# Kernel optimization log

Hardware: AMD Instinct MI355X
Metric: run time of the kernel (lower is better)

Reference implementation:

```python
import jax, jax.numpy as jnp
import numpy as np

B, N, D, H = 2, 2048, 1024, 16
HD = D // H  # head dim = 64
SCALING = (D / H) ** 0.5  # sqrt(64) = 8
EPS = 1e-5


def setup_inputs() -> dict:
    key = jax.random.key(0)
    k1, k2, k3 = jax.random.split(key, 3)
    return {
        "z": jax.random.normal(k1, (B, N, D), dtype=jnp.float32),
        "ln_scale": jnp.ones((D,), dtype=jnp.float32),
        "ln_bias": jnp.zeros((D,), dtype=jnp.float32),
        "w_qkv": jax.random.normal(k2, (D, 3 * D), dtype=jnp.float32) * (D ** -0.5),
        "w_proj": jax.random.normal(k3, (D, D), dtype=jnp.float32) * (D ** -0.5),
        "b_proj": jnp.zeros((D,), dtype=jnp.float32),
    }


def reference(z, ln_scale, ln_bias, w_qkv, w_proj, b_proj):
    b, n, d = z.shape
    # LayerNorm (pre-norm)
    mu = jnp.mean(z, axis=-1, keepdims=True)
    var = jnp.mean(jnp.square(z - mu), axis=-1, keepdims=True)
    zn = (z - mu) / jnp.sqrt(var + EPS) * ln_scale + ln_bias
    # QKV projection: [b, n, 3D]
    qkv = zn @ w_qkv
    # einops 'b n (h d qkv_n) -> qkv_n b h n d': qkv index is innermost
    qkv5 = qkv.reshape(b, n, H, HD, 3)  # [b, n, h, d, 3]
    q = jnp.transpose(qkv5[..., 0], (0, 2, 1, 3))  # [b, h, n, d]
    k = jnp.transpose(qkv5[..., 1], (0, 2, 1, 3))
    v = jnp.transpose(qkv5[..., 2], (0, 2, 1, 3))
    # Attention: scores scaled AFTER the matmul, as in the source
    scores = jnp.einsum('bhqd,bhkd->bhqk', q, k) / SCALING
    att = jax.nn.softmax(scores, axis=-1)
    out = jnp.einsum('bhal,bhlv->bhav', att, v)  # [b, h, n, d]
    out = jnp.transpose(out, (0, 2, 1, 3)).reshape(b, n, d)  # merge heads
    out = out @ w_proj + b_proj  # projection (dropout p=0)
    return z + out
```

## Files before the change

kernel.cpp:

```cpp
#include <hip/hip_runtime.h>
#include <stdint.h>
#include <math.h>

typedef unsigned short u16;
typedef float f32x4 __attribute__((ext_vector_type(4)));
typedef __bf16 bf16x8 __attribute__((ext_vector_type(8)));

__device__ __forceinline__ u16 f2bf(float f) {
    union { float f; uint32_t u; } c; c.f = f;
    return (u16)((c.u + 0x7FFFu + ((c.u >> 16) & 1u)) >> 16);
}

__device__ __forceinline__ void gload_lds16(const void* g, void* l) {
    __builtin_amdgcn_global_load_lds(
        (const __attribute__((address_space(1))) unsigned int*)g,
        (__attribute__((address_space(3))) unsigned int*)l, 16, 0, 0);
}

__global__ __launch_bounds__(256) void prep_kernel(const float* __restrict__ z,
                                                   const float* __restrict__ sc,
                                                   const float* __restrict__ bs,
                                                   const float* __restrict__ w_qkv,
                                                   const float* __restrict__ w_proj,
                                                   u16* __restrict__ zn,
                                                   u16* __restrict__ wqkvT,
                                                   u16* __restrict__ wprojT) {
    __shared__ float t[32][33];
    const int tid = threadIdx.x;
    const int bid = blockIdx.x;

    if (bid < 4096) {
        float* red = &t[0][0];
        const int row = bid;
        const float4 v = ((const float4*)(z + (size_t)row * 1024))[tid];
        float s = v.x + v.y + v.z + v.w;
        #pragma unroll
        for (int off = 32; off > 0; off >>= 1) s += __shfl_xor(s, off);
        if ((tid & 63) == 0) red[tid >> 6] = s;
        __syncthreads();
        const float mean = (red[0] + red[1] + red[2] + red[3]) * (1.0f / 1024.0f);
        const float dx = v.x - mean, dy = v.y - mean, dz = v.z - mean, dw = v.w - mean;
        float q = dx * dx + dy * dy + dz * dz + dw * dw;
        #pragma unroll
        for (int off = 32; off > 0; off >>= 1) q += __shfl_xor(q, off);
        if ((tid & 63) == 0) red[4 + (tid >> 6)] = q;
        __syncthreads();
        const float var = (red[4] + red[5] + red[6] + red[7]) * (1.0f / 1024.0f);
        const float rstd = rsqrtf(var + 1e-5f);
        const float4 scv = ((const float4*)sc)[tid];
        const float4 bsv = ((const float4*)bs)[tid];
        const u16 o0 = f2bf(dx * rstd * scv.x + bsv.x);
        const u16 o1 = f2bf(dy * rstd * scv.y + bsv.y);
        const u16 o2 = f2bf(dz * rstd * scv.z + bsv.z);
        const u16 o3 = f2bf(dw * rstd * scv.w + bsv.w);
        uint2 pk;
        pk.x = (uint32_t)o0 | ((uint32_t)o1 << 16);
        pk.y = (uint32_t)o2 | ((uint32_t)o3 << 16);
        *(uint2*)&zn[(size_t)row * 1024 + tid * 4] = pk;
        return;
    }

    const float* in;
    u16* out;
    int K, N, permute, bx, by;
    if (bid < 4096 + 3072) {
        const int r = bid - 4096;
        in = w_qkv; out = wqkvT; K = 1024; N = 3072; permute = 1;
        bx = r % 96; by = r / 96;
    } else {
        const int r = bid - 4096 - 3072;
        in = w_proj; out = wprojT; K = 1024; N = 1024; permute = 0;
        bx = r % 32; by = r / 32;
    }
    const int j = tid & 31, i0 = tid >> 5;
    const int kb = by * 32, nb = bx * 32;
    #pragma unroll
    for (int p = 0; p < 4; ++p) {
        int r = i0 + p * 8;
        t[r][j] = in[(size_t)(kb + r) * N + nb + j];
    }
    __syncthreads();
    #pragma unroll
    for (int p = 0; p < 4; ++p) {
        int r = i0 + p * 8;
        int c = nb + r;
        int np = c;
        if (permute) {
            int h = c / 192, rem = c - h * 192;
            int d = rem / 3, s = rem - d * 3;
            np = s * 1024 + h * 64 + d;
        }
        out[(size_t)np * K + kb + j] = f2bf(t[j][r]);
    }
}

__global__ __launch_bounds__(256, 3) void gemm_qkv(const u16* __restrict__ A,
                                                   const u16* __restrict__ Bt,
                                                   u16* __restrict__ qbuf,
                                                   u16* __restrict__ kbuf,
                                                   u16* __restrict__ vT) {
    __shared__ __align__(16) u16 sm[64 * 136];
    u16* const As = sm;
    u16* const Bs = sm + 4096;
    const int tid = threadIdx.x;
    const int wave = tid >> 6, lane = tid & 63;
    const int quad = lane >> 4, l16 = lane & 15;
    const int wm = (wave >> 1) * 64, wn = (wave & 1) * 64;
    const int row0 = blockIdx.x * 128, col0 = blockIdx.y * 128;
    const int gr = lane >> 2, gc = (lane & 3) * 8;
    f32x4 acc[4][4] = {};
    for (int kt = 0; kt < 1024; kt += 32) {
        __syncthreads();
        #pragma unroll
        for (int i = 0; i < 2; ++i) {
            const int rb = wave * 16 + i * 64;
            gload_lds16(&A[(size_t)(row0 + rb + gr) * 1024 + kt + gc], &As[rb * 32]);
            gload_lds16(&Bt[(size_t)(col0 + rb + gr) * 1024 + kt + gc], &Bs[rb * 32]);
        }
        __syncthreads();
        bf16x8 ax[4], bx[4];
        #pragma unroll
        for (int t = 0; t < 4; ++t) {
            ax[t] = *(const bf16x8*)&As[(wm + t * 16 + l16) * 32 + quad * 8];
            bx[t] = *(const bf16x8*)&Bs[(wn + t * 16 + l16) * 32 + quad * 8];
        }
        #pragma unroll
        for (int mt = 0; mt < 4; ++mt)
            #pragma unroll
            for (int nt = 0; nt < 4; ++nt)
                acc[mt][nt] = __builtin_amdgcn_mfma_f32_16x16x32_bf16(ax[mt], bx[nt], acc[mt][nt], 0, 0, 0);
    }
    const int s = col0 >> 10;
    if (s < 2) {
        u16* const dst = (s == 0) ? qbuf : kbuf;
        const float scl = (s == 0) ? 0.125f * 1.44269504088896f : 1.0f;
        #pragma unroll
        for (int mt = 0; mt < 4; ++mt) {
            #pragma unroll
            for (int nt = 0; nt < 4; ++nt) {
                #pragma unroll
                for (int e = 0; e < 4; ++e) {
                    const int row = row0 + wm + mt * 16 + quad * 4 + e;
                    const int col = col0 + wn + nt * 16 + l16;
                    const int b = row >> 11, n = row & 2047;
                    const int h = (col >> 6) & 15, d = col & 63;
                    dst[((size_t)(b * 16 + h) * 2048 + n) * 64 + d] = f2bf(acc[mt][nt][e] * scl);
                }
            }
        }
    } else {
        const int b = row0 >> 11, n0 = row0 & 2047;
        const int h0 = (col0 >> 6) & 15;
        for (int hh = 0; hh < 2; ++hh) {
            __syncthreads();
            if ((wave & 1) == hh) {
                #pragma unroll
                for (int mt = 0; mt < 4; ++mt) {
                    const int rl = wm + mt * 16 + quad * 4;
                    #pragma unroll
                    for (int nt = 0; nt < 4; ++nt) {
                        const int cl = nt * 16 + l16;
                        u16 tmp[4];
                        #pragma unroll
                        for (int e = 0; e < 4; ++e) tmp[e] = f2bf(acc[mt][nt][e]);
                        *(uint2*)&sm[cl * 136 + rl] = *(const uint2*)tmp;
                    }
                }
            }
            __syncthreads();
            const int bh = b * 16 + h0 + hh;
            #pragma unroll
            for (int pass = 0; pass < 4; ++pass) {
                const int chunk = pass * 256 + tid;
                const int d = chunk >> 4;
                const int nc = chunk & 15;
                const uint4 vv = *(const uint4*)&sm[d * 136 + nc * 8];
                *(uint4*)&vT[((size_t)bh * 64 + d) * 2048 + n0 + nc * 8] = vv;
            }
        }
    }
}

__global__ __launch_bounds__(512, 2) void attn_kernel(const u16* __restrict__ qb,
                                                      const u16* __restrict__ kb,
                                                      const u16* __restrict__ vT,
                                                      u16* __restrict__ att_out) {
    __shared__ __align__(16) char lds_raw[71680];
    u16* const smem0 = (u16*)lds_raw;
    const int tid = threadIdx.x;
    const int wave = tid >> 6, lane = tid & 63;
    const int quad = lane >> 4, l16 = lane & 15;
    const int kw = wave & 3, qw = wave >> 2;
    const int qt = blockIdx.x, bh = blockIdx.y;
    const int b = bh >> 4, h = bh & 15;

    bf16x8 qf[4][2];
    #pragma unroll
    for (int g = 0; g < 4; ++g) {
        const u16* qrow = &qb[(size_t)(bh * 2048 + qt * 128 + qw * 64 + g * 16 + l16) * 64];
        qf[g][0] = *(const bf16x8*)&qrow[quad * 8];
        qf[g][1] = *(const bf16x8*)&qrow[32 + quad * 8];
    }

    const u16* ksrc[2];
    const u16* vsrc[2];
    int kofs[2], vofs[2];
    #pragma unroll
    for (int j = 0; j < 2; ++j) {
        const int p = 8 * wave + 64 * j + (lane >> 3);
        const int kr = (p & 0x60) | ((p & 12) << 1) | ((p & 16) >> 2) | (p & 3);
        const int gk = (lane & 7) ^ (p & 7);
        ksrc[j] = kb + ((size_t)bh * 2048 + kr) * 64 + gk * 8;
        kofs[j] = (8 * wave + 64 * j) * 64;
        const int d = 4 * wave + 32 * j + (lane >> 4);
        const int gv = (lane & 15) ^ (d & 15);
        vsrc[j] = vT + ((size_t)bh * 64 + d) * 2048 + gv * 8;
        vofs[j] = 8192 + (4 * wave + 32 * j) * 128;
    }

    f32x4 o[4][4] = {};
    f32x4 l[4] = {};
    bf16x8 ones;
    #pragma unroll
    for (int i = 0; i < 8; ++i) ones[i] = (__bf16)1.0f;

    #pragma unroll
    for (int j = 0; j < 2; ++j) {
        gload_lds16(ksrc[j], smem0 + kofs[j]);
        gload_lds16(vsrc[j], smem0 + vofs[j]);
        ksrc[j] += 128 * 64;
        vsrc[j] += 128;
    }

    for (int kt = 0; kt < 16; ++kt) {
        __syncthreads();
        if (kt < 15) {
            u16* nb_ = smem0 + ((kt + 1) & 1) * 16384;
            #pragma unroll
            for (int j = 0; j < 2; ++j) {
                gload_lds16(ksrc[j], nb_ + kofs[j]);
                gload_lds16(vsrc[j], nb_ + vofs[j]);
                ksrc[j] += 128 * 64;
                vsrc[j] += 128;
            }
        }
        const u16* Ks = smem0 + (kt & 1) * 16384;
        const u16* Vs = Ks + 8192;

        f32x4 s[2][4] = {};
        __builtin_amdgcn_s_setprio(1);
        #pragma unroll
        for (int mtl = 0; mtl < 2; ++mtl) {
            const int r = kw * 32 + mtl * 16 + l16;
            const bf16x8 k0 = *(const bf16x8*)&Ks[r * 64 + (((quad) ^ (r & 7)) << 3)];
            const bf16x8 k1 = *(const bf16x8*)&Ks[r * 64 + (((quad + 4) ^ (r & 7)) << 3)];
            #pragma unroll
            for (int g = 0; g < 4; ++g) {
                s[mtl][g] = __builtin_amdgcn_mfma_f32_16x16x32_bf16(k0, qf[g][0], s[mtl][g], 0, 0, 0);
                s[mtl][g] = __builtin_amdgcn_mfma_f32_16x16x32_bf16(k1, qf[g][1], s[mtl][g], 0, 0, 0);
            }
        }
        __builtin_amdgcn_s_setprio(0);

        bf16x8 ap[4];
        #pragma unroll
        for (int g = 0; g < 4; ++g)
            #pragma unroll
            for (int mtl = 0; mtl < 2; ++mtl)
                #pragma unroll
                for (int e = 0; e < 4; ++e)
                    ap[g][mtl * 4 + e] = (__bf16)__builtin_amdgcn_exp2f(s[mtl][g][e]);

        __builtin_amdgcn_s_setprio(1);
        #pragma unroll
        for (int vt = 0; vt < 4; ++vt) {
            const int dd = vt * 16 + l16;
            const bf16x8 vf = *(const bf16x8*)&Vs[dd * 128 + (((kw * 4 + quad) ^ l16) << 3)];
            #pragma unroll
            for (int g = 0; g < 4; ++g)
                o[g][vt] = __builtin_amdgcn_mfma_f32_16x16x32_bf16(ap[g], vf, o[g][vt], 0, 0, 0);
        }
        #pragma unroll
        for (int g = 0; g < 4; ++g)
            l[g] = __builtin_amdgcn_mfma_f32_16x16x32_bf16(ap[g], ones, l[g], 0, 0, 0);
        __builtin_amdgcn_s_setprio(0);
    }

    float* const red = (float*)lds_raw;
    float* const lred = (float*)(lds_raw + 69632);
    #pragma unroll
    for (int qg = 0; qg < 2; ++qg) {
        __syncthreads();
        if (qw == qg) {
            #pragma unroll
            for (int g = 0; g < 4; ++g) {
                #pragma unroll
                for (int vt = 0; vt < 4; ++vt)
                    #pragma unroll
                    for (int e = 0; e < 4; ++e)
                        red[(kw * 64 + g * 16 + quad * 4 + e) * 68 + vt * 16 + l16] = o[g][vt][e];
                if (l16 == 0) {
                    #pragma unroll
                    for (int e = 0; e < 4; ++e)
                        lred[kw * 64 + g * 16 + quad * 4 + e] = l[g][e];
                }
            }
        }
        __syncthreads();
        #pragma unroll
        for (int rep = 0; rep < 2; ++rep) {
            const int idx = rep * 512 + tid;
            const int q = idx >> 4, dc = idx & 15;
            const f32x4 a0 = *(const f32x4*)&red[(0 * 64 + q) * 68 + dc * 4];
            const f32x4 a1 = *(const f32x4*)&red[(1 * 64 + q) * 68 + dc * 4];
            const f32x4 a2 = *(const f32x4*)&red[(2 * 64 + q) * 68 + dc * 4];
            const f32x4 a3 = *(const f32x4*)&red[(3 * 64 + q) * 68 + dc * 4];
            const f32x4 ss = a0 + a1 + a2 + a3;
            const float li = lred[q] + lred[64 + q] + lred[128 + q] + lred[192 + q];
            const float inv = 1.0f / li;
            u16 pk[4];
            #pragma unroll
            for (int e = 0; e < 4; ++e) pk[e] = f2bf(ss[e] * inv);
            const int qrow = qt * 128 + qg * 64 + q;
            *(uint2*)&att_out[(size_t)(b * 2048 + qrow) * 1024 + h * 64 + dc * 4] = *(const uint2*)pk;
        }
    }
}

__global__ __launch_bounds__(256) void gemm_proj(const u16* __restrict__ A,
                                                 const u16* __restrict__ Bt,
                                                 const float* __restrict__ bias,
                                                 const float* __restrict__ z,
                                                 float* __restrict__ out) {
    __shared__ __align__(16) u16 As[64 * 32];
    __shared__ __align__(16) u16 Bs[128 * 32];
    const int tid = threadIdx.x;
    const int wave = tid >> 6, lane = tid & 63;
    const int quad = lane >> 4, l16 = lane & 15;
    const int wm = (wave >> 1) * 32, wn = (wave & 1) * 64;
    const int row0 = blockIdx.x * 64, col0 = blockIdx.y * 128;
    const int gr = lane >> 2, gc = (lane & 3) * 8;
    f32x4 acc[2][4] = {};
    for (int kt = 0; kt < 1024; kt += 32) {
        __syncthreads();
        gload_lds16(&A[(size_t)(row0 + wave * 16 + gr) * 1024 + kt + gc], &As[(wave * 16) * 32]);
        #pragma unroll
        for (int i = 0; i < 2; ++i) {
            const int rb = wave * 16 + i * 64;
            gload_lds16(&Bt[(size_t)(col0 + rb + gr) * 1024 + kt + gc], &Bs[rb * 32]);
        }
        __syncthreads();
        bf16x8 ax[2], bx[4];
        #pragma unroll
        for (int t = 0; t < 2; ++t)
            ax[t] = *(const bf16x8*)&As[(wm + t * 16 + l16) * 32 + quad * 8];
        #pragma unroll
        for (int t = 0; t < 4; ++t)
            bx[t] = *(const bf16x8*)&Bs[(wn + t * 16 + l16) * 32 + quad * 8];
        #pragma unroll
        for (int mt = 0; mt < 2; ++mt)
            #pragma unroll
            for (int nt = 0; nt < 4; ++nt)
                acc[mt][nt] = __builtin_amdgcn_mfma_f32_16x16x32_bf16(ax[mt], bx[nt], acc[mt][nt], 0, 0, 0);
    }
    #pragma unroll
    for (int mt = 0; mt < 2; ++mt) {
        #pragma unroll
        for (int nt = 0; nt < 4; ++nt) {
            #pragma unroll
            for (int e = 0; e < 4; ++e) {
                const int row = row0 + wm + mt * 16 + quad * 4 + e;
                const int col = col0 + wn + nt * 16 + l16;
                out[(size_t)row * 1024 + col] = acc[mt][nt][e] + bias[col] + z[(size_t)row * 1024 + col];
            }
        }
    }
}

extern "C" void kernel_launch(void* const* d_in, const int* in_sizes, int n_in,
                              void* d_out, int out_size, void* d_ws, size_t ws_size,
                              hipStream_t stream) {
    const float* z        = (const float*)d_in[0];
    const float* ln_scale = (const float*)d_in[1];
    const float* ln_bias  = (const float*)d_in[2];
    const float* w_qkv    = (const float*)d_in[3];
    const float* w_proj   = (const float*)d_in[4];
    const float* b_proj   = (const float*)d_in[5];
    float* out = (float*)d_out;

    char* ws = (char*)d_ws;
    u16* zn     = (u16*)(ws);
    u16* wqkvT  = (u16*)(ws + (8u << 20));
    u16* wprojT = (u16*)(ws + (14u << 20));
    u16* qbuf   = (u16*)(ws + (16u << 20));
    u16* kbuf   = (u16*)(ws + (24u << 20));
    u16* vT     = (u16*)(ws + (32u << 20));
    u16* att_o  = (u16*)(ws + (40u << 20));

    prep_kernel<<<dim3(4096 + 3072 + 1024), 256, 0, stream>>>(
        z, ln_scale, ln_bias, w_qkv, w_proj, zn, wqkvT, wprojT);
    gemm_qkv<<<dim3(32, 24), 256, 0, stream>>>(zn, wqkvT, qbuf, kbuf, vT);
    attn_kernel<<<dim3(16, 32), 512, 0, stream>>>(qbuf, kbuf, vT, att_o);
    gemm_proj<<<dim3(64, 8), 256, 0, stream>>>(att_o, wprojT, b_proj, z, out);
}
```

Measured before the change: 180.3 us.

## Enlarge attention query tile to 256 with 2-way KV split and triple buffering

```diff
diff --git a/kernel.cpp b/kernel.cpp
--- a/kernel.cpp
+++ b/kernel.cpp
@@ -185,19 +185,19 @@
                                                       const u16* __restrict__ kb,
                                                       const u16* __restrict__ vT,
                                                       u16* __restrict__ att_out) {
-    __shared__ __align__(16) char lds_raw[71680];
+    __shared__ __align__(16) char lds_raw[98304];
     u16* const smem0 = (u16*)lds_raw;
     const int tid = threadIdx.x;
     const int wave = tid >> 6, lane = tid & 63;
     const int quad = lane >> 4, l16 = lane & 15;
-    const int kw = wave & 3, qw = wave >> 2;
+    const int kw = wave & 1, qw = wave >> 1;
     const int qt = blockIdx.x, bh = blockIdx.y;
     const int b = bh >> 4, h = bh & 15;
 
     bf16x8 qf[4][2];
     #pragma unroll
     for (int g = 0; g < 4; ++g) {
-        const u16* qrow = &qb[(size_t)(bh * 2048 + qt * 128 + qw * 64 + g * 16 + l16) * 64];
+        const u16* qrow = &qb[(size_t)(bh * 2048 + qt * 256 + qw * 64 + g * 16 + l16) * 64];
         qf[g][0] = *(const bf16x8*)&qrow[quad * 8];
         qf[g][1] = *(const bf16x8*)&qrow[32 + quad * 8];
     }
@@ -224,105 +224,105 @@
     #pragma unroll
     for (int i = 0; i < 8; ++i) ones[i] = (__bf16)1.0f;
 
-    #pragma unroll
-    for (int j = 0; j < 2; ++j) {
-        gload_lds16(ksrc[j], smem0 + kofs[j]);
-        gload_lds16(vsrc[j], smem0 + vofs[j]);
-        ksrc[j] += 128 * 64;
-        vsrc[j] += 128;
-    }
+    auto stage = [&](int buf) {
+        u16* dst = smem0 + buf * 16384;
+        #pragma unroll
+        for (int j = 0; j < 2; ++j) {
+            gload_lds16(ksrc[j], dst + kofs[j]);
+            gload_lds16(vsrc[j], dst + vofs[j]);
+            ksrc[j] += 128 * 64;
+            vsrc[j] += 128;
+        }
+    };
+    stage(0);
+    stage(1);
 
     for (int kt = 0; kt < 16; ++kt) {
-        __syncthreads();
-        if (kt < 15) {
-            u16* nb_ = smem0 + ((kt + 1) & 1) * 16384;
-            #pragma unroll
-            for (int j = 0; j < 2; ++j) {
-                gload_lds16(ksrc[j], nb_ + kofs[j]);
-                gload_lds16(vsrc[j], nb_ + vofs[j]);
-                ksrc[j] += 128 * 64;
-                vsrc[j] += 128;
-            }
-        }
-        const u16* Ks = smem0 + (kt & 1) * 16384;
+        if (kt < 15) asm volatile("s_waitcnt vmcnt(4)\n\ts_barrier" ::: "memory");
+        else         asm volatile("s_waitcnt vmcnt(0)\n\ts_barrier" ::: "memory");
+        if (kt <= 13) stage((kt + 2) % 3);
+
+        const u16* Ks = smem0 + (kt % 3) * 16384;
         const u16* Vs = Ks + 8192;
 
-        f32x4 s[2][4] = {};
-        __builtin_amdgcn_s_setprio(1);
-        #pragma unroll
-        for (int mtl = 0; mtl < 2; ++mtl) {
-            const int r = kw * 32 + mtl * 16 + l16;
-            const bf16x8 k0 = *(const bf16x8*)&Ks[r * 64 + (((quad) ^ (r & 7)) << 3)];
-            const bf16x8 k1 = *(const bf16x8*)&Ks[r * 64 + (((quad + 4) ^ (r & 7)) << 3)];
-            #pragma unroll
-            for (int g = 0; g < 4; ++g) {
-                s[mtl][g] = __builtin_amdgcn_mfma_f32_16x16x32_bf16(k0, qf[g][0], s[mtl][g], 0, 0, 0);
-                s[mtl][g] = __builtin_amdgcn_mfma_f32_16x16x32_bf16(k1, qf[g][1], s[mtl][g], 0, 0, 0);
-            }
-        }
-        __builtin_amdgcn_s_setprio(0);
-
-        bf16x8 ap[4];
-        #pragma unroll
-        for (int g = 0; g < 4; ++g)
-            #pragma unroll
-            for (int mtl = 0; mtl < 2; ++mtl)
-                #pragma unroll
-                for (int e = 0; e < 4; ++e)
-                    ap[g][mtl * 4 + e] = (__bf16)__builtin_amdgcn_exp2f(s[mtl][g][e]);
+        bf16x8 ap[4][2];
+        #pragma unroll
+        for (int f = 0; f < 2; ++f) {
+            f32x4 s2[2][4] = {};
+            #pragma unroll
+            for (int m2 = 0; m2 < 2; ++m2) {
+                const int r = kw * 64 + (f * 2 + m2) * 16 + l16;
+                const bf16x8 k0 = *(const bf16x8*)&Ks[r * 64 + ((quad ^ (r & 7)) << 3)];
+                const bf16x8 k1 = *(const bf16x8*)&Ks[r * 64 + (((quad + 4) ^ (r & 7)) << 3)];
+                #pragma unroll
+                for (int g = 0; g < 4; ++g) {
+                    s2[m2][g] = __builtin_amdgcn_mfma_f32_16x16x32_bf16(k0, qf[g][0], s2[m2][g], 0, 0, 0);
+                    s2[m2][g] = __builtin_amdgcn_mfma_f32_16x16x32_bf16(k1, qf[g][1], s2[m2][g], 0, 0, 0);
+                }
+            }
+            #pragma unroll
+            for (int g = 0; g < 4; ++g)
+                #pragma unroll
+                for (int m2 = 0; m2 < 2; ++m2)
+                    #pragma unroll
+                    for (int e = 0; e < 4; ++e)
+                        ap[g][f][m2 * 4 + e] = (__bf16)__builtin_amdgcn_exp2f(s2[m2][g][e]);
+        }
 
         __builtin_amdgcn_s_setprio(1);
         #pragma unroll
         for (int vt = 0; vt < 4; ++vt) {
             const int dd = vt * 16 + l16;
-            const bf16x8 vf = *(const bf16x8*)&Vs[dd * 128 + (((kw * 4 + quad) ^ l16) << 3)];
-            #pragma unroll
-            for (int g = 0; g < 4; ++g)
-                o[g][vt] = __builtin_amdgcn_mfma_f32_16x16x32_bf16(ap[g], vf, o[g][vt], 0, 0, 0);
-        }
-        #pragma unroll
-        for (int g = 0; g < 4; ++g)
-            l[g] = __builtin_amdgcn_mfma_f32_16x16x32_bf16(ap[g], ones, l[g], 0, 0, 0);
+            #pragma unroll
+            for (int f = 0; f < 2; ++f) {
+                const int c = kw * 2 + f;
+                const bf16x8 vf = *(const bf16x8*)&Vs[dd * 128 + (((c * 4 + quad) ^ l16) << 3)];
+                #pragma unroll
+                for (int g = 0; g < 4; ++g)
+                    o[g][vt] = __builtin_amdgcn_mfma_f32_16x16x32_bf16(ap[g][f], vf, o[g][vt], 0, 0, 0);
+            }
+        }
+        #pragma unroll
+        for (int g = 0; g < 4; ++g) {
+            l[g] = __builtin_amdgcn_mfma_f32_16x16x32_bf16(ap[g][0], ones, l[g], 0, 0, 0);
+            l[g] = __builtin_amdgcn_mfma_f32_16x16x32_bf16(ap[g][1], ones, l[g], 0, 0, 0);
+        }
         __builtin_amdgcn_s_setprio(0);
     }
 
+    __syncthreads();
     float* const red = (float*)lds_raw;
     float* const lred = (float*)(lds_raw + 69632);
-    #pragma unroll
-    for (int qg = 0; qg < 2; ++qg) {
-        __syncthreads();
-        if (qw == qg) {
-            #pragma unroll
-            for (int g = 0; g < 4; ++g) {
-                #pragma unroll
-                for (int vt = 0; vt < 4; ++vt)
-                    #pragma unroll
-                    for (int e = 0; e < 4; ++e)
-                        red[(kw * 64 + g * 16 + quad * 4 + e) * 68 + vt * 16 + l16] = o[g][vt][e];
-                if (l16 == 0) {
-                    #pragma unroll
-                    for (int e = 0; e < 4; ++e)
-                        lred[kw * 64 + g * 16 + quad * 4 + e] = l[g][e];
+    if (kw == 1) {
+        #pragma unroll
+        for (int g = 0; g < 4; ++g) {
+            #pragma unroll
+            for (int vt = 0; vt < 4; ++vt)
+                #pragma unroll
+                for (int e = 0; e < 4; ++e)
+                    red[(qw * 64 + g * 16 + quad * 4 + e) * 68 + vt * 16 + l16] = o[g][vt][e];
+            if (l16 == 0) {
+                #pragma unroll
+                for (int e = 0; e < 4; ++e)
+                    lred[qw * 64 + g * 16 + quad * 4 + e] = l[g][e];
+            }
+        }
+    }
+    __syncthreads();
+    if (kw == 0) {
+        #pragma unroll
+        for (int g = 0; g < 4; ++g) {
+            #pragma unroll
+            for (int e = 0; e < 4; ++e) {
+                const float li = lred[qw * 64 + g * 16 + quad * 4 + e] + l[g][e];
+                const float inv = 1.0f / li;
+                const int row = qt * 256 + qw * 64 + g * 16 + quad * 4 + e;
+                #pragma unroll
+                for (int vt = 0; vt < 4; ++vt) {
+                    const float sum = red[(qw * 64 + g * 16 + quad * 4 + e) * 68 + vt * 16 + l16] + o[g][vt][e];
+                    att_out[(size_t)(b * 2048 + row) * 1024 + h * 64 + vt * 16 + l16] = f2bf(sum * inv);
                 }
             }
-        }
-        __syncthreads();
-        #pragma unroll
-        for (int rep = 0; rep < 2; ++rep) {
-            const int idx = rep * 512 + tid;
-            const int q = idx >> 4, dc = idx & 15;
-            const f32x4 a0 = *(const f32x4*)&red[(0 * 64 + q) * 68 + dc * 4];
-            const f32x4 a1 = *(const f32x4*)&red[(1 * 64 + q) * 68 + dc * 4];
-            const f32x4 a2 = *(const f32x4*)&red[(2 * 64 + q) * 68 + dc * 4];
-            const f32x4 a3 = *(const f32x4*)&red[(3 * 64 + q) * 68 + dc * 4];
-            const f32x4 ss = a0 + a1 + a2 + a3;
-            const float li = lred[q] + lred[64 + q] + lred[128 + q] + lred[192 + q];
-            const float inv = 1.0f / li;
-            u16 pk[4];
-            #pragma unroll
-            for (int e = 0; e < 4; ++e) pk[e] = f2bf(ss[e] * inv);
-            const int qrow = qt * 128 + qg * 64 + q;
-            *(uint2*)&att_out[(size_t)(b * 2048 + qrow) * 1024 + h * 64 + dc * 4] = *(const uint2*)pk;
         }
     }
 }
@@ -400,6 +400,6 @@
     prep_kernel<<<dim3(4096 + 3072 + 1024), 256, 0, stream>>>(
         z, ln_scale, ln_bias, w_qkv, w_proj, zn, wqkvT, wprojT);
     gemm_qkv<<<dim3(32, 24), 256, 0, stream>>>(zn, wqkvT, qbuf, kbuf, vT);
-    attn_kernel<<<dim3(16, 32), 512, 0, stream>>>(qbuf, kbuf, vT, att_o);
+    attn_kernel<<<dim3(8, 32), 512, 0, stream>>>(qbuf, kbuf, vT, att_o);
     gemm_proj<<<dim3(64, 8), 256, 0, stream>>>(att_o, wprojT, b_proj, z, out);
 }
```

Result: no change. 179.7 us (-0.3%).
